# Optimization experiments

Measured on AMD Instinct MI355X. Metric: run time of the kernel, lower is better.

Reference implementation:

```python
import jax, jax.numpy as jnp
import numpy as np

K = 5  # number of nearest neighbors (module default)


def setup_inputs() -> dict:
    key = jax.random.key(0)
    k1, k2 = jax.random.split(key)
    source_pc = jax.random.normal(k1, (2, 8192, 3), dtype=jnp.float32)
    target_pc = jax.random.normal(k2, (2, 8192, 3), dtype=jnp.float32)
    return {"source_pc": source_pc, "target_pc": target_pc}


def _valid_mask(pc_flat):
    # point is valid if any coordinate is nonzero (move_zero_point)
    return jnp.any(pc_flat != 0.0, axis=-1)


def reference(source_pc, target_pc):
    # move_zero_point flattens all batches into one batch-1 cloud; we emulate
    # the filtering with masks (invalid targets -> +inf distance, invalid
    # sources excluded from the mean) to stay jit-compatible.
    src = source_pc.reshape(-1, 3)   # [Ms, 3] query points
    tgt = target_pc.reshape(-1, 3)   # [Nt, 3] reference points
    src_mask = _valid_mask(src)      # [Ms]
    tgt_mask = _valid_mask(tgt)      # [Nt]

    # squared pairwise distances: |s|^2 + |t|^2 - 2 s.t  -> [Ms, Nt]
    s2 = jnp.sum(src * src, axis=-1)[:, None]
    t2 = jnp.sum(tgt * tgt, axis=-1)[None, :]
    d2 = s2 + t2 - 2.0 * jnp.einsum('md,nd->mn', src, tgt)
    d = jnp.sqrt(jnp.maximum(d2, 1e-12))

    BIG = jnp.float32(1e10)
    d = jnp.where(tgt_mask[None, :], d, BIG)  # drop zero target points

    # k smallest distances per source point (knn returns Euclidean dists)
    neg_topk, _ = jax.lax.top_k(-d, K)        # [Ms, K]
    knn_d = -neg_topk

    # mean over valid source points only
    w = src_mask.astype(knn_d.dtype)
    total = jnp.sum(knn_d * w[:, None])
    count = jnp.sum(w) * K
    return total / count
```

## Files before the change

kernel.cpp:

```cpp
#include <hip/hip_runtime.h>
#include <math.h>

#define KNN 5
#define BLOCK 256
#define TILE_T 2048
#define WAVES_PER_BLOCK (BLOCK / 64)
#define SRCW 8
#define SRC_PER_BLOCK (WAVES_PER_BLOCK * SRCW)
#define NSPLIT 2

__device__ __forceinline__ float vmin(float a, float b) {
    float r;
    asm("v_min_f32 %0, %1, %2" : "=v"(r) : "v"(a), "v"(b));
    return r;
}
__device__ __forceinline__ float vmax(float a, float b) {
    float r;
    asm("v_max_f32 %0, %1, %2" : "=v"(r) : "v"(a), "v"(b));
    return r;
}

#define INS5(K0, K1, K2, K3, K4, V)                                       \
    do {                                                                  \
        float _v = (V);                                                   \
        K4 = __builtin_amdgcn_fmed3f(K3, K4, _v);                         \
        K3 = __builtin_amdgcn_fmed3f(K2, K3, _v);                         \
        K2 = __builtin_amdgcn_fmed3f(K1, K2, _v);                         \
        K1 = __builtin_amdgcn_fmed3f(K0, K1, _v);                         \
        K0 = vmin(K0, _v);                                                \
    } while (0)

#define MERGE55(a0, a1, a2, a3, a4, b0, b1, b2, b3, b4)                   \
    do {                                                                  \
        float r0 = vmin(a0, b0);                                          \
        float r1 = vmin(vmin(a1, b1), vmax(a0, b0));                      \
        float r2 = vmin(vmin(a2, b2), vmin(vmax(a0, b1), vmax(a1, b0)));  \
        float r3 = vmin(vmin(a3, b3),                                     \
                        vmin(vmax(a0, b2), vmin(vmax(a1, b1), vmax(a2, b0)))); \
        float r4 = vmin(vmin(a4, b4),                                     \
                        vmin(vmin(vmax(a0, b3), vmax(a1, b2)),            \
                             vmin(vmax(a2, b1), vmax(a3, b0))));          \
        a0 = r0; a1 = r1; a2 = r2; a3 = r3; a4 = r4;                      \
    } while (0)


__global__ void init_acc_kernel(float* acc) {
    acc[0] = 0.0f;
    acc[1] = 0.0f;
}

__global__ void finalize_kernel(const float* acc, float* out) {
    out[0] = acc[0] / (acc[1] * (float)KNN);
}


__global__ __launch_bounds__(BLOCK, 4) void knn_split_kernel(
        const float* __restrict__ src, const float* __restrict__ tgt,
        float* __restrict__ partials, int ms, int nt, int nth, int spad) {
    __shared__ __align__(16) float xs[TILE_T];
    __shared__ __align__(16) float ys[TILE_T];
    __shared__ __align__(16) float zs[TILE_T];
    __shared__ __align__(16) float w2[TILE_T];

    const int tid = threadIdx.x;
    const int wv = tid >> 6;
    const int lane = tid & 63;
    const int sbase = (blockIdx.x * WAVES_PER_BLOCK + wv) * SRCW;
    const int half = blockIdx.y;
    const int hbase = half * nth;
    const int hend = min(nt, hbase + nth);

    float nx[SRCW], ny[SRCW], nz[SRCW];
#pragma unroll
    for (int s = 0; s < SRCW; ++s) {
        int sp = sbase + s;
        float x = 0.0f, y = 0.0f, z = 0.0f;
        if (sp < ms) {
            x = src[3 * sp + 0];
            y = src[3 * sp + 1];
            z = src[3 * sp + 2];
        }
        nx[s] = -2.0f * x;
        ny[s] = -2.0f * y;
        nz[s] = -2.0f * z;
    }

    float q0[SRCW], q1[SRCW], q2[SRCW], q3[SRCW], q4[SRCW];
#pragma unroll
    for (int s = 0; s < SRCW; ++s) {
        q0[s] = 1e30f; q1[s] = 1e30f; q2[s] = 1e30f; q3[s] = 1e30f; q4[s] = 1e30f;
    }

    for (int t0 = hbase; t0 < hend; t0 += TILE_T) {
        if (t0 + TILE_T <= hend) {
#pragma unroll
            for (int cc = 0; cc < TILE_T / 4; cc += BLOCK) {
                int c = cc + tid;
                const float4* t4 = reinterpret_cast<const float4*>(tgt + (size_t)t0 * 3);
                float4 f0 = t4[3 * c + 0];
                float4 f1 = t4[3 * c + 1];
                float4 f2 = t4[3 * c + 2];
                float px[4] = {f0.x, f0.w, f1.z, f2.y};
                float py[4] = {f0.y, f1.x, f1.w, f2.z};
                float pz[4] = {f0.z, f1.y, f2.x, f2.w};
                float pw[4];
#pragma unroll
                for (int j = 0; j < 4; ++j) {
                    bool v = (px[j] != 0.0f) || (py[j] != 0.0f) || (pz[j] != 0.0f);
                    if (!v) { px[j] = 1e10f; py[j] = 0.0f; pz[j] = 0.0f; }
                    pw[j] = fmaf(px[j], px[j], fmaf(py[j], py[j], pz[j] * pz[j]));
                }
                int t = 4 * c;
                *reinterpret_cast<float4*>(&xs[t]) = make_float4(px[0], px[1], px[2], px[3]);
                *reinterpret_cast<float4*>(&ys[t]) = make_float4(py[0], py[1], py[2], py[3]);
                *reinterpret_cast<float4*>(&zs[t]) = make_float4(pz[0], pz[1], pz[2], pz[3]);
                *reinterpret_cast<float4*>(&w2[t]) = make_float4(pw[0], pw[1], pw[2], pw[3]);
            }
        } else {
            int cnt = hend - t0;
            for (int t = tid; t < TILE_T; t += BLOCK) {
                float x = 1e10f, y = 0.0f, z = 0.0f;
                if (t < cnt) {
                    x = tgt[3 * (size_t)(t0 + t) + 0];
                    y = tgt[3 * (size_t)(t0 + t) + 1];
                    z = tgt[3 * (size_t)(t0 + t) + 2];
                    if (x == 0.0f && y == 0.0f && z == 0.0f) { x = 1e10f; y = 0.0f; z = 0.0f; }
                }
                xs[t] = x; ys[t] = y; zs[t] = z;
                w2[t] = fmaf(x, x, fmaf(y, y, z * z));
            }
        }
        __syncthreads();

#pragma unroll 2
        for (int i = 0; i < TILE_T / 256; ++i) {
            int t = (i << 8) + (lane << 2);
            float4 x4 = *reinterpret_cast<const float4*>(&xs[t]);
            float4 y4 = *reinterpret_cast<const float4*>(&ys[t]);
            float4 z4 = *reinterpret_cast<const float4*>(&zs[t]);
            float4 w4 = *reinterpret_cast<const float4*>(&w2[t]);
#pragma unroll
            for (int s = 0; s < SRCW; ++s) {
                float qa = fmaf(nx[s], x4.x, fmaf(ny[s], y4.x, fmaf(nz[s], z4.x, w4.x)));
                float qb = fmaf(nx[s], x4.y, fmaf(ny[s], y4.y, fmaf(nz[s], z4.y, w4.y)));
                float qc = fmaf(nx[s], x4.z, fmaf(ny[s], y4.z, fmaf(nz[s], z4.z, w4.z)));
                float qd = fmaf(nx[s], x4.w, fmaf(ny[s], y4.w, fmaf(nz[s], z4.w, w4.w)));
                INS5(q0[s], q1[s], q2[s], q3[s], q4[s], qa);
                INS5(q0[s], q1[s], q2[s], q3[s], q4[s], qb);
                INS5(q0[s], q1[s], q2[s], q3[s], q4[s], qc);
                INS5(q0[s], q1[s], q2[s], q3[s], q4[s], qd);
            }
        }
        __syncthreads();
    }

#pragma unroll
    for (int off = 32; off >= 1; off >>= 1) {
#pragma unroll
        for (int s = 0; s < SRCW; ++s) {
            float b0 = __shfl_xor(q0[s], off);
            float b1 = __shfl_xor(q1[s], off);
            float b2 = __shfl_xor(q2[s], off);
            float b3 = __shfl_xor(q3[s], off);
            float b4 = __shfl_xor(q4[s], off);
            MERGE55(q0[s], q1[s], q2[s], q3[s], q4[s], b0, b1, b2, b3, b4);
        }
    }

    if (lane == 0) {
        float* base = partials + ((size_t)half * spad + sbase) * 8;
#pragma unroll
        for (int s = 0; s < SRCW; ++s) {
            if (sbase + s < ms) {
                *reinterpret_cast<float4*>(base + 8 * s) =
                    make_float4(q0[s], q1[s], q2[s], q3[s]);
                *reinterpret_cast<float4*>(base + 8 * s + 4) =
                    make_float4(q4[s], 0.0f, 0.0f, 0.0f);
            }
        }
    }
}


__global__ __launch_bounds__(BLOCK) void merge_kernel(
        const float* __restrict__ src, const float* __restrict__ partials,
        float* __restrict__ acc, int ms, int spad) {
    __shared__ float red_s[WAVES_PER_BLOCK];
    __shared__ float red_c[WAVES_PER_BLOCK];

    const int tid = threadIdx.x;
    const int sp = blockIdx.x * BLOCK + tid;

    float ssum = 0.0f, scnt = 0.0f;
    if (sp < ms) {
        const float* r0p = partials + (size_t)sp * 8;
        const float* r1p = partials + ((size_t)spad + sp) * 8;
        float4 lo0 = *reinterpret_cast<const float4*>(r0p);
        float a4 = r0p[4];
        float4 lo1 = *reinterpret_cast<const float4*>(r1p);
        float b4 = r1p[4];
        float a0 = lo0.x, a1 = lo0.y, a2 = lo0.z, a3 = lo0.w;
        MERGE55(a0, a1, a2, a3, a4, lo1.x, lo1.y, lo1.z, lo1.w, b4);

        float x = src[3 * sp + 0];
        float y = src[3 * sp + 1];
        float z = src[3 * sp + 2];
        bool valid = (x != 0.0f) || (y != 0.0f) || (z != 0.0f);
        float s2 = fmaf(x, x, fmaf(y, y, z * z));
        if (valid) {
            ssum = sqrtf(fmaxf(a0 + s2, 1e-12f)) + sqrtf(fmaxf(a1 + s2, 1e-12f)) +
                   sqrtf(fmaxf(a2 + s2, 1e-12f)) + sqrtf(fmaxf(a3 + s2, 1e-12f)) +
                   sqrtf(fmaxf(a4 + s2, 1e-12f));
            scnt = 1.0f;
        }
    }

#pragma unroll
    for (int off = 32; off >= 1; off >>= 1) {
        ssum += __shfl_down(ssum, off);
        scnt += __shfl_down(scnt, off);
    }
    if ((tid & 63) == 0) {
        red_s[tid >> 6] = ssum;
        red_c[tid >> 6] = scnt;
    }
    __syncthreads();
    if (tid == 0) {
        float s = 0.0f, c = 0.0f;
#pragma unroll
        for (int i = 0; i < WAVES_PER_BLOCK; ++i) { s += red_s[i]; c += red_c[i]; }
        atomicAdd(&acc[0], s);
        atomicAdd(&acc[1], c);
    }
}


__global__ __launch_bounds__(BLOCK) void knn_mono_kernel(
        const float* __restrict__ src, const float* __restrict__ tgt,
        float* __restrict__ acc, int ms, int nt) {
    __shared__ __align__(16) float xs[TILE_T];
    __shared__ __align__(16) float ys[TILE_T];
    __shared__ __align__(16) float zs[TILE_T];
    __shared__ __align__(16) float w2[TILE_T];
    __shared__ float red_s[WAVES_PER_BLOCK];
    __shared__ float red_c[WAVES_PER_BLOCK];

    const int tid = threadIdx.x;
    const int wv = tid >> 6;
    const int lane = tid & 63;
    const int sbase = (blockIdx.x * WAVES_PER_BLOCK + wv) * 4;

    float nx[4], ny[4], nz[4], s2a[4], svalid[4];
#pragma unroll
    for (int s = 0; s < 4; ++s) {
        int sp = sbase + s;
        float x = 0.0f, y = 0.0f, z = 0.0f;
        if (sp < ms) {
            x = src[3 * sp + 0]; y = src[3 * sp + 1]; z = src[3 * sp + 2];
        }
        svalid[s] = (sp < ms && (x != 0.0f || y != 0.0f || z != 0.0f)) ? 1.0f : 0.0f;
        nx[s] = -2.0f * x; ny[s] = -2.0f * y; nz[s] = -2.0f * z;
        s2a[s] = fmaf(x, x, fmaf(y, y, z * z));
    }
    float q0[4], q1[4], q2[4], q3[4], q4[4];
#pragma unroll
    for (int s = 0; s < 4; ++s) {
        q0[s] = 1e30f; q1[s] = 1e30f; q2[s] = 1e30f; q3[s] = 1e30f; q4[s] = 1e30f;
    }
    for (int t0 = 0; t0 < nt; t0 += TILE_T) {
        int cnt = min(TILE_T, nt - t0);
        for (int t = tid; t < TILE_T; t += BLOCK) {
            float x = 1e10f, y = 0.0f, z = 0.0f;
            if (t < cnt) {
                x = tgt[3 * (size_t)(t0 + t) + 0];
                y = tgt[3 * (size_t)(t0 + t) + 1];
                z = tgt[3 * (size_t)(t0 + t) + 2];
                if (x == 0.0f && y == 0.0f && z == 0.0f) { x = 1e10f; y = 0.0f; z = 0.0f; }
            }
            xs[t] = x; ys[t] = y; zs[t] = z;
            w2[t] = fmaf(x, x, fmaf(y, y, z * z));
        }
        __syncthreads();
#pragma unroll 2
        for (int i = 0; i < TILE_T / 256; ++i) {
            int t = (i << 8) + (lane << 2);
            float4 x4 = *reinterpret_cast<const float4*>(&xs[t]);
            float4 y4 = *reinterpret_cast<const float4*>(&ys[t]);
            float4 z4 = *reinterpret_cast<const float4*>(&zs[t]);
            float4 w4 = *reinterpret_cast<const float4*>(&w2[t]);
#pragma unroll
            for (int s = 0; s < 4; ++s) {
                float qa = fmaf(nx[s], x4.x, fmaf(ny[s], y4.x, fmaf(nz[s], z4.x, w4.x)));
                float qb = fmaf(nx[s], x4.y, fmaf(ny[s], y4.y, fmaf(nz[s], z4.y, w4.y)));
                float qc = fmaf(nx[s], x4.z, fmaf(ny[s], y4.z, fmaf(nz[s], z4.z, w4.z)));
                float qd = fmaf(nx[s], x4.w, fmaf(ny[s], y4.w, fmaf(nz[s], z4.w, w4.w)));
                INS5(q0[s], q1[s], q2[s], q3[s], q4[s], qa);
                INS5(q0[s], q1[s], q2[s], q3[s], q4[s], qb);
                INS5(q0[s], q1[s], q2[s], q3[s], q4[s], qc);
                INS5(q0[s], q1[s], q2[s], q3[s], q4[s], qd);
            }
        }
        __syncthreads();
    }
#pragma unroll
    for (int off = 32; off >= 1; off >>= 1) {
#pragma unroll
        for (int s = 0; s < 4; ++s) {
            float b0 = __shfl_xor(q0[s], off);
            float b1 = __shfl_xor(q1[s], off);
            float b2 = __shfl_xor(q2[s], off);
            float b3 = __shfl_xor(q3[s], off);
            float b4 = __shfl_xor(q4[s], off);
            MERGE55(q0[s], q1[s], q2[s], q3[s], q4[s], b0, b1, b2, b3, b4);
        }
    }
    if (lane == 0) {
        float ssum = 0.0f, scnt = 0.0f;
#pragma unroll
        for (int s = 0; s < 4; ++s) {
            float d0 = sqrtf(fmaxf(q0[s] + s2a[s], 1e-12f));
            float d1 = sqrtf(fmaxf(q1[s] + s2a[s], 1e-12f));
            float d2 = sqrtf(fmaxf(q2[s] + s2a[s], 1e-12f));
            float d3 = sqrtf(fmaxf(q3[s] + s2a[s], 1e-12f));
            float d4 = sqrtf(fmaxf(q4[s] + s2a[s], 1e-12f));
            ssum += svalid[s] * (d0 + d1 + d2 + d3 + d4);
            scnt += svalid[s];
        }
        red_s[wv] = ssum;
        red_c[wv] = scnt;
    }
    __syncthreads();
    if (tid == 0) {
        float s = 0.0f, c = 0.0f;
#pragma unroll
        for (int i = 0; i < WAVES_PER_BLOCK; ++i) { s += red_s[i]; c += red_c[i]; }
        atomicAdd(&acc[0], s);
        atomicAdd(&acc[1], c);
    }
}


extern "C" void kernel_launch(void* const* d_in, const int* in_sizes, int n_in,
                              void* d_out, int out_size, void* d_ws, size_t ws_size,
                              hipStream_t stream) {
    const float* src = (const float*)d_in[0];
    const float* tgt = (const float*)d_in[1];
    const int ms = in_sizes[0] / 3;
    const int nt = in_sizes[1] / 3;

    float* acc = (float*)d_ws;
    init_acc_kernel<<<1, 1, 0, stream>>>(acc);

    const int ngroups = (ms + SRC_PER_BLOCK - 1) / SRC_PER_BLOCK;
    const int spad = ngroups * SRC_PER_BLOCK;
    int nth = (nt + NSPLIT - 1) / NSPLIT;
    nth = (nth + TILE_T - 1) / TILE_T * TILE_T;

    const size_t need = 16 + (size_t)NSPLIT * spad * 8 * sizeof(float);

    if (ws_size >= need) {
        float* partials = (float*)((char*)d_ws + 16);
        dim3 grid(ngroups, NSPLIT);
        knn_split_kernel<<<grid, BLOCK, 0, stream>>>(src, tgt, partials, ms, nt, nth, spad);
        merge_kernel<<<(ms + BLOCK - 1) / BLOCK, BLOCK, 0, stream>>>(src, partials, acc, ms, spad);
    } else {
        const int blocks = (ms + 15) / 16;
        knn_mono_kernel<<<blocks, BLOCK, 0, stream>>>(src, tgt, acc, ms, nt);
    }

    finalize_kernel<<<1, 1, 0, stream>>>(acc, (float*)d_out);
}
```

Before: 80.28 us.

## Replace brute-force KNN with uniform-grid spatial binning and ring search

Builds a 28^3 uniform grid over [-6,6]^3. Targets and sources are binned with count, scan and scatter kernels, and each source is handled by 16 lanes that search expanding shells of cells until the fifth-best distance is within the certified radius. This drops the all-pairs distance computation in favour of a mostly local search, which moves the work from compute-bound brute force to several small launches, atomics and irregular memory access. Correctness relies on the early-exit bound and on clamping out-of-range points into boundary cells. The fallback path also loses the monolithic kernel variant.

```diff
diff --git a/kernel.cpp b/kernel.cpp
--- a/kernel.cpp
+++ b/kernel.cpp
@@ -8,6 +8,14 @@
 #define SRCW 8
 #define SRC_PER_BLOCK (WAVES_PER_BLOCK * SRCW)
 #define NSPLIT 2
+
+#define G 28
+#define NC (G * G * G)
+#define GRANGE 6.0f
+#define H (2.0f * GRANGE / G)
+#define INVH ((float)G / (2.0f * GRANGE))
+#define SCHUNK 22
+#define LPS 16
 
 __device__ __forceinline__ float vmin(float a, float b) {
     float r;
@@ -44,13 +52,203 @@
     } while (0)
 
 
+__global__ void finalize_kernel(const float* acc, float* out) {
+    out[0] = acc[0] / (acc[1] * (float)KNN);
+}
+
 __global__ void init_acc_kernel(float* acc) {
     acc[0] = 0.0f;
     acc[1] = 0.0f;
 }
 
-__global__ void finalize_kernel(const float* acc, float* out) {
-    out[0] = acc[0] / (acc[1] * (float)KNN);
+
+__global__ void grid_init_kernel(int* cnt_t, int* cnt_s, float* acc, int nc) {
+    int i = blockIdx.x * blockDim.x + threadIdx.x;
+    if (i == 0) { acc[0] = 0.0f; acc[1] = 0.0f; }
+    for (; i < nc; i += gridDim.x * blockDim.x) {
+        cnt_t[i] = 0;
+        cnt_s[i] = 0;
+    }
+}
+
+__device__ __forceinline__ int cell_of(float x, float y, float z) {
+    int cx = (int)floorf((x + GRANGE) * INVH);
+    int cy = (int)floorf((y + GRANGE) * INVH);
+    int cz = (int)floorf((z + GRANGE) * INVH);
+    cx = min(max(cx, 0), G - 1);
+    cy = min(max(cy, 0), G - 1);
+    cz = min(max(cz, 0), G - 1);
+    return (cz * G + cy) * G + cx;
+}
+
+__global__ void bin_count_kernel(const float* __restrict__ src,
+                                 const float* __restrict__ tgt,
+                                 int ms, int nt,
+                                 int* __restrict__ cnt_s,
+                                 int* __restrict__ cnt_t) {
+    int i = blockIdx.x * blockDim.x + threadIdx.x;
+    int n = ms + nt;
+    for (; i < n; i += gridDim.x * blockDim.x) {
+        bool isT = (i >= ms);
+        const float* p = isT ? (tgt + 3 * (size_t)(i - ms)) : (src + 3 * (size_t)i);
+        float x = p[0], y = p[1], z = p[2];
+        if (isT && x == 0.0f && y == 0.0f && z == 0.0f) continue;
+        atomicAdd((isT ? cnt_t : cnt_s) + cell_of(x, y, z), 1);
+    }
+}
+
+__global__ __launch_bounds__(1024) void scan_kernel(int* cnt_t, int* off_t,
+                                                    int* cnt_s, int* off_s) {
+    __shared__ int psum[1024];
+    int* c = blockIdx.x ? cnt_s : cnt_t;
+    int* o = blockIdx.x ? off_s : off_t;
+    const int tid = threadIdx.x;
+    const int lo = tid * SCHUNK;
+
+    int buf[SCHUNK];
+    int s = 0;
+#pragma unroll
+    for (int j = 0; j < SCHUNK; ++j) {
+        int i = lo + j;
+        int v = (i < NC) ? c[i] : 0;
+        buf[j] = v;
+        s += v;
+    }
+    psum[tid] = s;
+    __syncthreads();
+    for (int d = 1; d < 1024; d <<= 1) {
+        int v = (tid >= d) ? psum[tid - d] : 0;
+        __syncthreads();
+        psum[tid] += v;
+        __syncthreads();
+    }
+    int run = tid ? psum[tid - 1] : 0;
+#pragma unroll
+    for (int j = 0; j < SCHUNK; ++j) {
+        int i = lo + j;
+        if (i < NC) {
+            o[i] = run;
+            c[i] = run;
+            run += buf[j];
+        }
+    }
+    if (tid == 1023) o[NC] = psum[1023];
+}
+
+__global__ void scatter_kernel(const float* __restrict__ src,
+                               const float* __restrict__ tgt,
+                               int ms, int nt,
+                               int* __restrict__ cur_s, int* __restrict__ cur_t,
+                               float4* __restrict__ pts_s,
+                               float4* __restrict__ pts_t) {
+    int i = blockIdx.x * blockDim.x + threadIdx.x;
+    int n = ms + nt;
+    for (; i < n; i += gridDim.x * blockDim.x) {
+        bool isT = (i >= ms);
+        const float* p = isT ? (tgt + 3 * (size_t)(i - ms)) : (src + 3 * (size_t)i);
+        float x = p[0], y = p[1], z = p[2];
+        if (isT && x == 0.0f && y == 0.0f && z == 0.0f) continue;
+        int cell = cell_of(x, y, z);
+        int slot = atomicAdd((isT ? cur_t : cur_s) + cell, 1);
+        float w = fmaf(x, x, fmaf(y, y, z * z));
+        (isT ? pts_t : pts_s)[slot] = make_float4(x, y, z, w);
+    }
+}
+
+__global__ __launch_bounds__(BLOCK) void knn_grid_kernel(
+        const float4* __restrict__ pts_s, const float4* __restrict__ pts_t,
+        const int* __restrict__ off_t, float* __restrict__ acc, int ms) {
+    __shared__ float red_s[BLOCK / LPS];
+    __shared__ float red_c[BLOCK / LPS];
+
+    const int tid = threadIdx.x;
+    const int g = tid / LPS;
+    const int m = tid % LPS;
+    const int sidx = blockIdx.x * (BLOCK / LPS) + g;
+    const bool live = (sidx < ms);
+
+    float4 sp = pts_s[live ? sidx : 0];
+    const float sx = sp.x, sy = sp.y, sz = sp.z, s2 = sp.w;
+    const float nx = -2.0f * sx, ny = -2.0f * sy, nz = -2.0f * sz;
+
+    int cx = (int)floorf((sx + GRANGE) * INVH);
+    int cy = (int)floorf((sy + GRANGE) * INVH);
+    int cz = (int)floorf((sz + GRANGE) * INVH);
+    cx = min(max(cx, 0), G - 1);
+    cy = min(max(cy, 0), G - 1);
+    cz = min(max(cz, 0), G - 1);
+
+    float q0 = 1e30f, q1 = 1e30f, q2 = 1e30f, q3 = 1e30f, q4 = 1e30f;
+
+    auto scan_row = [&](int cyy, int czz, int xlo, int xhi) {
+        if ((unsigned)cyy >= G || (unsigned)czz >= G) return;
+        xlo = max(xlo, 0);
+        xhi = min(xhi, G - 1);
+        if (xlo > xhi) return;
+        int base = (czz * G + cyy) * G;
+        int st = off_t[base + xlo];
+        int en = off_t[base + xhi + 1];
+        for (int i = st + m; i < en; i += LPS) {
+            float4 p = pts_t[i];
+            float q = fmaf(nx, p.x, fmaf(ny, p.y, fmaf(nz, p.z, p.w)));
+            INS5(q0, q1, q2, q3, q4, q);
+        }
+    };
+
+    float m0 = 1e30f, m1 = 1e30f, m2 = 1e30f, m3 = 1e30f, m4 = 1e30f;
+
+    scan_row(cy, cz, cx, cx);
+    for (int r = 1; r < G; ++r) {
+        for (int dz = -r; dz <= r; ++dz) {
+            int czz = cz + dz;
+            int adz = dz < 0 ? -dz : dz;
+            for (int dy = -r; dy <= r; ++dy) {
+                int cyy = cy + dy;
+                int ady = dy < 0 ? -dy : dy;
+                if (adz == r || ady == r) {
+                    scan_row(cyy, czz, cx - r, cx + r);
+                } else {
+                    scan_row(cyy, czz, cx - r, cx - r);
+                    scan_row(cyy, czz, cx + r, cx + r);
+                }
+            }
+        }
+        m0 = q0; m1 = q1; m2 = q2; m3 = q3; m4 = q4;
+#pragma unroll
+        for (int o = 1; o < LPS; o <<= 1) {
+            float b0 = __shfl_xor(m0, o);
+            float b1 = __shfl_xor(m1, o);
+            float b2 = __shfl_xor(m2, o);
+            float b3 = __shfl_xor(m3, o);
+            float b4 = __shfl_xor(m4, o);
+            MERGE55(m0, m1, m2, m3, m4, b0, b1, b2, b3, b4);
+        }
+        float rh = (float)r * H;
+        if (m4 <= fmaf(rh, rh, -s2)) break;
+    }
+
+    float ssum = 0.0f, scnt = 0.0f;
+    if (live && m == 0) {
+        bool valid = (sx != 0.0f) || (sy != 0.0f) || (sz != 0.0f);
+        if (valid) {
+            ssum = sqrtf(fmaxf(m0 + s2, 1e-12f)) + sqrtf(fmaxf(m1 + s2, 1e-12f)) +
+                   sqrtf(fmaxf(m2 + s2, 1e-12f)) + sqrtf(fmaxf(m3 + s2, 1e-12f)) +
+                   sqrtf(fmaxf(m4 + s2, 1e-12f));
+            scnt = 1.0f;
+        }
+    }
+    if (m == 0) {
+        red_s[g] = ssum;
+        red_c[g] = scnt;
+    }
+    __syncthreads();
+    if (tid == 0) {
+        float s = 0.0f, c = 0.0f;
+#pragma unroll
+        for (int i = 0; i < BLOCK / LPS; ++i) { s += red_s[i]; c += red_c[i]; }
+        atomicAdd(&acc[0], s);
+        atomicAdd(&acc[1], c);
+    }
 }
 
 
@@ -181,7 +379,6 @@
     }
 }
 
-
 __global__ __launch_bounds__(BLOCK) void merge_kernel(
         const float* __restrict__ src, const float* __restrict__ partials,
         float* __restrict__ acc, int ms, int spad) {
@@ -214,7 +411,6 @@
             scnt = 1.0f;
         }
     }
-
 #pragma unroll
     for (int off = 32; off >= 1; off >>= 1) {
         ssum += __shfl_down(ssum, off);
@@ -223,111 +419,6 @@
     if ((tid & 63) == 0) {
         red_s[tid >> 6] = ssum;
         red_c[tid >> 6] = scnt;
-    }
-    __syncthreads();
-    if (tid == 0) {
-        float s = 0.0f, c = 0.0f;
-#pragma unroll
-        for (int i = 0; i < WAVES_PER_BLOCK; ++i) { s += red_s[i]; c += red_c[i]; }
-        atomicAdd(&acc[0], s);
-        atomicAdd(&acc[1], c);
-    }
-}
-
-
-__global__ __launch_bounds__(BLOCK) void knn_mono_kernel(
-        const float* __restrict__ src, const float* __restrict__ tgt,
-        float* __restrict__ acc, int ms, int nt) {
-    __shared__ __align__(16) float xs[TILE_T];
-    __shared__ __align__(16) float ys[TILE_T];
-    __shared__ __align__(16) float zs[TILE_T];
-    __shared__ __align__(16) float w2[TILE_T];
-    __shared__ float red_s[WAVES_PER_BLOCK];
-    __shared__ float red_c[WAVES_PER_BLOCK];
-
-    const int tid = threadIdx.x;
-    const int wv = tid >> 6;
-    const int lane = tid & 63;
-    const int sbase = (blockIdx.x * WAVES_PER_BLOCK + wv) * 4;
-
-    float nx[4], ny[4], nz[4], s2a[4], svalid[4];
-#pragma unroll
-    for (int s = 0; s < 4; ++s) {
-        int sp = sbase + s;
-        float x = 0.0f, y = 0.0f, z = 0.0f;
-        if (sp < ms) {
-            x = src[3 * sp + 0]; y = src[3 * sp + 1]; z = src[3 * sp + 2];
-        }
-        svalid[s] = (sp < ms && (x != 0.0f || y != 0.0f || z != 0.0f)) ? 1.0f : 0.0f;
-        nx[s] = -2.0f * x; ny[s] = -2.0f * y; nz[s] = -2.0f * z;
-        s2a[s] = fmaf(x, x, fmaf(y, y, z * z));
-    }
-    float q0[4], q1[4], q2[4], q3[4], q4[4];
-#pragma unroll
-    for (int s = 0; s < 4; ++s) {
-        q0[s] = 1e30f; q1[s] = 1e30f; q2[s] = 1e30f; q3[s] = 1e30f; q4[s] = 1e30f;
-    }
-    for (int t0 = 0; t0 < nt; t0 += TILE_T) {
-        int cnt = min(TILE_T, nt - t0);
-        for (int t = tid; t < TILE_T; t += BLOCK) {
-            float x = 1e10f, y = 0.0f, z = 0.0f;
-            if (t < cnt) {
-                x = tgt[3 * (size_t)(t0 + t) + 0];
-                y = tgt[3 * (size_t)(t0 + t) + 1];
-                z = tgt[3 * (size_t)(t0 + t) + 2];
-                if (x == 0.0f && y == 0.0f && z == 0.0f) { x = 1e10f; y = 0.0f; z = 0.0f; }
-            }
-            xs[t] = x; ys[t] = y; zs[t] = z;
-            w2[t] = fmaf(x, x, fmaf(y, y, z * z));
-        }
-        __syncthreads();
-#pragma unroll 2
-        for (int i = 0; i < TILE_T / 256; ++i) {
-            int t = (i << 8) + (lane << 2);
-            float4 x4 = *reinterpret_cast<const float4*>(&xs[t]);
-            float4 y4 = *reinterpret_cast<const float4*>(&ys[t]);
-            float4 z4 = *reinterpret_cast<const float4*>(&zs[t]);
-            float4 w4 = *reinterpret_cast<const float4*>(&w2[t]);
-#pragma unroll
-            for (int s = 0; s < 4; ++s) {
-                float qa = fmaf(nx[s], x4.x, fmaf(ny[s], y4.x, fmaf(nz[s], z4.x, w4.x)));
-                float qb = fmaf(nx[s], x4.y, fmaf(ny[s], y4.y, fmaf(nz[s], z4.y, w4.y)));
-                float qc = fmaf(nx[s], x4.z, fmaf(ny[s], y4.z, fmaf(nz[s], z4.z, w4.z)));
-                float qd = fmaf(nx[s], x4.w, fmaf(ny[s], y4.w, fmaf(nz[s], z4.w, w4.w)));
-                INS5(q0[s], q1[s], q2[s], q3[s], q4[s], qa);
-                INS5(q0[s], q1[s], q2[s], q3[s], q4[s], qb);
-                INS5(q0[s], q1[s], q2[s], q3[s], q4[s], qc);
-                INS5(q0[s], q1[s], q2[s], q3[s], q4[s], qd);
-            }
-        }
-        __syncthreads();
-    }
-#pragma unroll
-    for (int off = 32; off >= 1; off >>= 1) {
-#pragma unroll
-        for (int s = 0; s < 4; ++s) {
-            float b0 = __shfl_xor(q0[s], off);
-            float b1 = __shfl_xor(q1[s], off);
-            float b2 = __shfl_xor(q2[s], off);
-            float b3 = __shfl_xor(q3[s], off);
-            float b4 = __shfl_xor(q4[s], off);
-            MERGE55(q0[s], q1[s], q2[s], q3[s], q4[s], b0, b1, b2, b3, b4);
-        }
-    }
-    if (lane == 0) {
-        float ssum = 0.0f, scnt = 0.0f;
-#pragma unroll
-        for (int s = 0; s < 4; ++s) {
-            float d0 = sqrtf(fmaxf(q0[s] + s2a[s], 1e-12f));
-            float d1 = sqrtf(fmaxf(q1[s] + s2a[s], 1e-12f));
-            float d2 = sqrtf(fmaxf(q2[s] + s2a[s], 1e-12f));
-            float d3 = sqrtf(fmaxf(q3[s] + s2a[s], 1e-12f));
-            float d4 = sqrtf(fmaxf(q4[s] + s2a[s], 1e-12f));
-            ssum += svalid[s] * (d0 + d1 + d2 + d3 + d4);
-            scnt += svalid[s];
-        }
-        red_s[wv] = ssum;
-        red_c[wv] = scnt;
     }
     __syncthreads();
     if (tid == 0) {
@@ -348,25 +439,43 @@
     const int ms = in_sizes[0] / 3;
     const int nt = in_sizes[1] / 3;
 
-    float* acc = (float*)d_ws;
-    init_acc_kernel<<<1, 1, 0, stream>>>(acc);
-
+    char* p = (char*)d_ws;
+    auto take = [&p](size_t bytes) {
+        char* r = p;
+        p += (bytes + 15) & ~(size_t)15;
+        return r;
+    };
+    float* acc   = (float*)take(2 * sizeof(float));
+    int* off_t   = (int*)take((NC + 1) * sizeof(int));
+    int* cnt_t   = (int*)take(NC * sizeof(int));
+    int* off_s   = (int*)take((NC + 1) * sizeof(int));
+    int* cnt_s   = (int*)take(NC * sizeof(int));
+    float4* pts_t = (float4*)take((size_t)nt * sizeof(float4));
+    float4* pts_s = (float4*)take((size_t)ms * sizeof(float4));
+    const size_t need_grid = (size_t)(p - (char*)d_ws);
+
+    if (ws_size >= need_grid) {
+        const int n = ms + nt;
+        grid_init_kernel<<<128, 256, 0, stream>>>(cnt_t, cnt_s, acc, NC);
+        bin_count_kernel<<<(n + 255) / 256, 256, 0, stream>>>(src, tgt, ms, nt, cnt_s, cnt_t);
+        scan_kernel<<<2, 1024, 0, stream>>>(cnt_t, off_t, cnt_s, off_s);
+        scatter_kernel<<<(n + 255) / 256, 256, 0, stream>>>(src, tgt, ms, nt,
+                                                            cnt_s, cnt_t, pts_s, pts_t);
+        const int qblocks = (ms + (BLOCK / LPS) - 1) / (BLOCK / LPS);
+        knn_grid_kernel<<<qblocks, BLOCK, 0, stream>>>(pts_s, pts_t, off_t, acc, ms);
+        finalize_kernel<<<1, 1, 0, stream>>>(acc, (float*)d_out);
+        return;
+    }
+
+    float* acc2 = (float*)d_ws;
+    init_acc_kernel<<<1, 1, 0, stream>>>(acc2);
     const int ngroups = (ms + SRC_PER_BLOCK - 1) / SRC_PER_BLOCK;
     const int spad = ngroups * SRC_PER_BLOCK;
     int nth = (nt + NSPLIT - 1) / NSPLIT;
     nth = (nth + TILE_T - 1) / TILE_T * TILE_T;
-
-    const size_t need = 16 + (size_t)NSPLIT * spad * 8 * sizeof(float);
-
-    if (ws_size >= need) {
-        float* partials = (float*)((char*)d_ws + 16);
-        dim3 grid(ngroups, NSPLIT);
-        knn_split_kernel<<<grid, BLOCK, 0, stream>>>(src, tgt, partials, ms, nt, nth, spad);
-        merge_kernel<<<(ms + BLOCK - 1) / BLOCK, BLOCK, 0, stream>>>(src, partials, acc, ms, spad);
-    } else {
-        const int blocks = (ms + 15) / 16;
-        knn_mono_kernel<<<blocks, BLOCK, 0, stream>>>(src, tgt, acc, ms, nt);
-    }
-
-    finalize_kernel<<<1, 1, 0, stream>>>(acc, (float*)d_out);
-}
+    float* partials = (float*)((char*)d_ws + 16);
+    dim3 grid(ngroups, NSPLIT);
+    knn_split_kernel<<<grid, BLOCK, 0, stream>>>(src, tgt, partials, ms, nt, nth, spad);
+    merge_kernel<<<(ms + BLOCK - 1) / BLOCK, BLOCK, 0, stream>>>(src, partials, acc2, ms, spad);
+    finalize_kernel<<<1, 1, 0, stream>>>(acc2, (float*)d_out);
+}
```

Result: slower. 150.8 us (+87.9%).
